# Kernel optimization log

Hardware: AMD Instinct MI355X
Metric: run time of the kernel (lower is better)

Reference implementation:

```python
import jax, jax.numpy as jnp
import numpy as np

B, S, D, L = 64, 4096, 256, 16

def setup_inputs() -> dict:
    key = jax.random.key(0)
    k1, k2, k3 = jax.random.split(key, 3)
    right_emb = jax.random.normal(k1, (B, S, D), dtype=jnp.float32)
    # pair_id in [-1, L): -1 means identity passthrough (as in the torch forward)
    pair_id = jax.random.randint(k2, (B, 1), -1, L, dtype=jnp.int32)
    # kaiming-uniform-ish random mapping matrices (reset_with_identity=False)
    mapping = jax.random.normal(k3, (L, D, D), dtype=jnp.float32) * (1.0 / np.sqrt(D))
    return {"right_emb": right_emb, "mapping": mapping, "pair_id": pair_id}

def reference(right_emb, mapping, pair_id):
    # lang id per sample; -1 -> passthrough
    lang = pair_id[:, 0]                      # [B]
    passthrough = lang < 0                    # [B] bool
    Wg = mapping[jnp.clip(lang, 0)]           # [B, D, D] gathered per-sample matrices
    # F.linear(x, W) == x @ W^T : out[b,s,e] = sum_d x[b,s,d] * W[b,e,d]
    out = jnp.einsum('bsd,bed->bse', right_emb, Wg)
    return jnp.where(passthrough[:, None, None], right_emb, out)
```

## Files before the change

kernel.cpp:

```cpp
#include <hip/hip_runtime.h>


typedef __attribute__((ext_vector_type(8))) short bf16x8;
typedef __attribute__((ext_vector_type(16))) float f32x16;

#define S_DIM 4096
#define D_DIM 256
#define BM 128
#define BN 256
#define BK 64
#define LDK 72
#define NT 256

static __device__ __forceinline__ unsigned short f2bf(float f) {
    unsigned int u = __float_as_uint(f);
    return (unsigned short)((u + 0x7fffu + ((u >> 16) & 1u)) >> 16);
}

__global__ void cvt_w_kernel(const float* __restrict__ w, unsigned short* __restrict__ wb) {
    int i = (blockIdx.x * 256 + threadIdx.x) * 4;
    float4 v = *(const float4*)(w + i);
    ushort4 p;
    p.x = f2bf(v.x); p.y = f2bf(v.y); p.z = f2bf(v.z); p.w = f2bf(v.w);
    *(ushort4*)(wb + i) = p;
}

__global__ __launch_bounds__(NT, 2) void MultipleMappings_5952824672291_kernel(
    const float* __restrict__ X, const unsigned short* __restrict__ Wb,
    const int* __restrict__ pair_id, float* __restrict__ Y)
{
    __shared__ unsigned short ldsA[BM * LDK];
    __shared__ unsigned short ldsW[BN * LDK];

    const int b = blockIdx.y;
    const int t = threadIdx.x;
    const long base = ((long)b * S_DIM + (long)blockIdx.x * BM) * D_DIM;
    const float* Xb = X + base;
    float* Yb = Y + base;
    const int lang = pair_id[b];

    if (lang < 0) {
        #pragma unroll
        for (int i = 0; i < 32; ++i) {
            int f4 = t + i * NT;
            *(float4*)(Yb + (long)f4 * 4) = *(const float4*)(Xb + (long)f4 * 4);
        }
        return;
    }

    const unsigned short* Wl = Wb + (size_t)lang * (D_DIM * D_DIM);

    const int lane  = t & 63;
    const int wave  = t >> 6;
    const int wr    = wave >> 1;
    const int wc    = wave & 1;
    const int lrow  = lane & 31;
    const int khalf = lane >> 5;

    f32x16 acc[2][4] = {};

    for (int kc = 0; kc < 4; ++kc) {
        __syncthreads();
        #pragma unroll
        for (int i = 0; i < 8; ++i) {
            int flat = t + i * NT;
            int row = flat >> 4, c4 = flat & 15;
            float4 v = *(const float4*)(Xb + row * D_DIM + kc * BK + c4 * 4);
            ushort4 p;
            p.x = f2bf(v.x); p.y = f2bf(v.y); p.z = f2bf(v.z); p.w = f2bf(v.w);
            *(ushort4*)&ldsA[row * LDK + c4 * 4] = p;
        }
        #pragma unroll
        for (int i = 0; i < 8; ++i) {
            int flat = t + i * NT;
            int row = flat >> 3, c8 = flat & 7;
            bf16x8 v = *(const bf16x8*)(Wl + row * D_DIM + kc * BK + c8 * 8);
            *(bf16x8*)&ldsW[row * LDK + c8 * 8] = v;
        }
        __syncthreads();
        #pragma unroll
        for (int kk = 0; kk < 4; ++kk) {
            int k = kk * 16 + khalf * 8;
            bf16x8 af[2], bfr[4];
            #pragma unroll
            for (int rt = 0; rt < 2; ++rt)
                af[rt] = *(const bf16x8*)&ldsA[(wr * 64 + rt * 32 + lrow) * LDK + k];
            #pragma unroll
            for (int ct = 0; ct < 4; ++ct)
                bfr[ct] = *(const bf16x8*)&ldsW[(wc * 128 + ct * 32 + lrow) * LDK + k];
            #pragma unroll
            for (int rt = 0; rt < 2; ++rt)
                #pragma unroll
                for (int ct = 0; ct < 4; ++ct)
                    acc[rt][ct] = __builtin_amdgcn_mfma_f32_32x32x16_bf16(
                        af[rt], bfr[ct], acc[rt][ct], 0, 0, 0);
        }
    }

    #pragma unroll
    for (int rt = 0; rt < 2; ++rt) {
        #pragma unroll
        for (int ct = 0; ct < 4; ++ct) {
            const int colg = wc * 128 + ct * 32 + lrow;
            #pragma unroll
            for (int r = 0; r < 16; ++r) {
                int rowg = wr * 64 + rt * 32 + 4 * khalf + (r & 3) + 8 * (r >> 2);
                Yb[(long)rowg * D_DIM + colg] = acc[rt][ct][r];
            }
        }
    }
}

extern "C" void kernel_launch(void* const* d_in, const int* in_sizes, int n_in,
                              void* d_out, int out_size, void* d_ws, size_t ws_size,
                              hipStream_t stream) {
    const float* X   = (const float*)d_in[0];
    const float* W   = (const float*)d_in[1];
    const int*   pid = (const int*)d_in[2];
    float*       Y   = (float*)d_out;
    unsigned short* Wbf = (unsigned short*)d_ws;

    cvt_w_kernel<<<dim3(1024), dim3(256), 0, stream>>>(W, Wbf);

    dim3 grid(S_DIM / BM, 64);
    MultipleMappings_5952824672291_kernel<<<grid, dim3(NT), 0, stream>>>(X, Wbf, pid, Y);
}
```

Baseline: 445.4 us.

## Load X and W straight into LDS with swizzled layout and halve row tile

Both the fp32 activation tile and the bf16 weight tile are now copied from global memory directly into LDS with global_load_lds 16-byte transfers, so they no longer pass through registers. The fp32-to-bf16 conversion of X moves to the LDS read just before each MFMA. Row padding is replaced by an XOR swizzle so the direct copies stay contiguous while LDS bank conflicts are avoided. The row tile drops from 128 to 64 and launch bounds rise to 3 blocks per CU, which raises occupancy but doubles how often the weight matrix is reloaded per block and adds conversion work on the MFMA path.

```diff
diff --git a/kernel.cpp b/kernel.cpp
--- a/kernel.cpp
+++ b/kernel.cpp
@@ -6,15 +6,26 @@
 
 #define S_DIM 4096
 #define D_DIM 256
-#define BM 128
-#define BN 256
+#define BM 64
 #define BK 64
-#define LDK 72
 #define NT 256
 
 static __device__ __forceinline__ unsigned short f2bf(float f) {
     unsigned int u = __float_as_uint(f);
     return (unsigned short)((u + 0x7fffu + ((u >> 16) & 1u)) >> 16);
+}
+
+static __device__ __forceinline__ unsigned int pack_bf2(float lo, float hi) {
+    unsigned int a = __float_as_uint(lo), b = __float_as_uint(hi);
+    a += 0x7fffu + ((a >> 16) & 1u);
+    b += 0x7fffu + ((b >> 16) & 1u);
+    return (a >> 16) | (b & 0xffff0000u);
+}
+
+static __device__ __forceinline__ void dma16(const void* g, void* l) {
+    __builtin_amdgcn_global_load_lds(
+        (const __attribute__((address_space(1))) unsigned int*)g,
+        (__attribute__((address_space(3))) unsigned int*)l, 16, 0, 0);
 }
 
 __global__ void cvt_w_kernel(const float* __restrict__ w, unsigned short* __restrict__ wb) {
@@ -25,12 +36,12 @@
     *(ushort4*)(wb + i) = p;
 }
 
-__global__ __launch_bounds__(NT, 2) void MultipleMappings_5952824672291_kernel(
+__global__ __launch_bounds__(NT, 3) void MultipleMappings_5952824672291_kernel(
     const float* __restrict__ X, const unsigned short* __restrict__ Wb,
     const int* __restrict__ pair_id, float* __restrict__ Y)
 {
-    __shared__ unsigned short ldsA[BM * LDK];
-    __shared__ unsigned short ldsW[BN * LDK];
+    __shared__ unsigned short ldsW[256 * 64];
+    __shared__ float ldsA[64 * 64];
 
     const int b = blockIdx.y;
     const int t = threadIdx.x;
@@ -41,7 +52,7 @@
 
     if (lang < 0) {
         #pragma unroll
-        for (int i = 0; i < 32; ++i) {
+        for (int i = 0; i < 16; ++i) {
             int f4 = t + i * NT;
             *(float4*)(Yb + (long)f4 * 4) = *(const float4*)(Xb + (long)f4 * 4);
         }
@@ -57,56 +68,55 @@
     const int lrow  = lane & 31;
     const int khalf = lane >> 5;
 
-    f32x16 acc[2][4] = {};
+    f32x16 acc[4] = {};
 
     for (int kc = 0; kc < 4; ++kc) {
         __syncthreads();
         #pragma unroll
-        for (int i = 0; i < 8; ++i) {
-            int flat = t + i * NT;
-            int row = flat >> 4, c4 = flat & 15;
-            float4 v = *(const float4*)(Xb + row * D_DIM + kc * BK + c4 * 4);
-            ushort4 p;
-            p.x = f2bf(v.x); p.y = f2bf(v.y); p.z = f2bf(v.z); p.w = f2bf(v.w);
-            *(ushort4*)&ldsA[row * LDK + c4 * 4] = p;
+        for (int j = 0; j < 8; ++j) {
+            int slot = j * NT + t;
+            int row = slot >> 3, kgl = slot & 7;
+            int kgs = kgl ^ (row & 7);
+            dma16(Wl + row * D_DIM + kc * BK + kgs * 8, (char*)ldsW + slot * 16);
         }
         #pragma unroll
-        for (int i = 0; i < 8; ++i) {
-            int flat = t + i * NT;
-            int row = flat >> 3, c8 = flat & 7;
-            bf16x8 v = *(const bf16x8*)(Wl + row * D_DIM + kc * BK + c8 * 8);
-            *(bf16x8*)&ldsW[row * LDK + c8 * 8] = v;
+        for (int j = 0; j < 4; ++j) {
+            int slot = j * NT + t;
+            int row = slot >> 4, kgl = slot & 15;
+            int kgs = kgl ^ (row & 15);
+            dma16(Xb + row * D_DIM + kc * BK + kgs * 4, (char*)ldsA + slot * 16);
         }
         __syncthreads();
         #pragma unroll
         for (int kk = 0; kk < 4; ++kk) {
-            int k = kk * 16 + khalf * 8;
-            bf16x8 af[2], bfr[4];
+            const int k = kk * 16 + khalf * 8;
+            const int arow = wr * 32 + lrow;
+            const int am = arow & 15;
+            const int kg0 = k >> 2;
+            float4 a0 = *(const float4*)((char*)ldsA + arow * 256 + ((kg0 ^ am) * 16));
+            float4 a1 = *(const float4*)((char*)ldsA + arow * 256 + (((kg0 + 1) ^ am) * 16));
+            union { bf16x8 v; unsigned int u[4]; } af;
+            af.u[0] = pack_bf2(a0.x, a0.y);
+            af.u[1] = pack_bf2(a0.z, a0.w);
+            af.u[2] = pack_bf2(a1.x, a1.y);
+            af.u[3] = pack_bf2(a1.z, a1.w);
+            const int kg = k >> 3;
             #pragma unroll
-            for (int rt = 0; rt < 2; ++rt)
-                af[rt] = *(const bf16x8*)&ldsA[(wr * 64 + rt * 32 + lrow) * LDK + k];
-            #pragma unroll
-            for (int ct = 0; ct < 4; ++ct)
-                bfr[ct] = *(const bf16x8*)&ldsW[(wc * 128 + ct * 32 + lrow) * LDK + k];
-            #pragma unroll
-            for (int rt = 0; rt < 2; ++rt)
-                #pragma unroll
-                for (int ct = 0; ct < 4; ++ct)
-                    acc[rt][ct] = __builtin_amdgcn_mfma_f32_32x32x16_bf16(
-                        af[rt], bfr[ct], acc[rt][ct], 0, 0, 0);
+            for (int ct = 0; ct < 4; ++ct) {
+                const int brow = wc * 128 + ct * 32 + lrow;
+                bf16x8 bfv = *(const bf16x8*)((char*)ldsW + brow * 128 + ((kg ^ (brow & 7)) * 16));
+                acc[ct] = __builtin_amdgcn_mfma_f32_32x32x16_bf16(af.v, bfv, acc[ct], 0, 0, 0);
+            }
         }
     }
 
     #pragma unroll
-    for (int rt = 0; rt < 2; ++rt) {
+    for (int ct = 0; ct < 4; ++ct) {
+        const int colg = wc * 128 + ct * 32 + lrow;
         #pragma unroll
-        for (int ct = 0; ct < 4; ++ct) {
-            const int colg = wc * 128 + ct * 32 + lrow;
-            #pragma unroll
-            for (int r = 0; r < 16; ++r) {
-                int rowg = wr * 64 + rt * 32 + 4 * khalf + (r & 3) + 8 * (r >> 2);
-                Yb[(long)rowg * D_DIM + colg] = acc[rt][ct][r];
-            }
+        for (int r = 0; r < 16; ++r) {
+            int rowg = wr * 32 + 4 * khalf + (r & 3) + 8 * (r >> 2);
+            Yb[(long)rowg * D_DIM + colg] = acc[ct][r];
         }
     }
 }
```

Result: no change. 442.9 us (-0.6%).
